# Kernel optimization log

Measured on AMD Instinct MI355X. Metric: run time of the kernel, lower is better.

## Reference

```python
import jax, jax.numpy as jnp
import numpy as np
import math

DIM, DEPTH, HEADS, VOCAB, DMODEL = 200, 6, 10, 7, 512
DH = DIM // HEADS                      # 20
NBF = int(DH * math.log(DH))           # 59 FAVOR+ random features
FF = 4 * DIM                           # 800


def setup_inputs() -> dict:
    key = jax.random.key(0)
    ks = iter(jax.random.split(key, 32))
    s = 0.02
    inp = {
        'x': jax.random.normal(next(ks), (4, 16, 2048), jnp.float32),
        'token_emb': jax.random.normal(next(ks), (VOCAB, DIM)) * s,
        'ln1_g': jnp.ones((DEPTH, DIM)), 'ln1_b': jnp.zeros((DEPTH, DIM)),
        'wq': jax.random.normal(next(ks), (DEPTH, DIM, DIM)) * s, 'bq': jnp.zeros((DEPTH, DIM)),
        'wk': jax.random.normal(next(ks), (DEPTH, DIM, DIM)) * s, 'bk': jnp.zeros((DEPTH, DIM)),
        'wv': jax.random.normal(next(ks), (DEPTH, DIM, DIM)) * s, 'bv': jnp.zeros((DEPTH, DIM)),
        'proj': jax.random.normal(next(ks), (DEPTH, NBF, DH)),  # FAVOR+ projection (buffer)
        'wo': jax.random.normal(next(ks), (DEPTH, DIM, DIM)) * s, 'bo': jnp.zeros((DEPTH, DIM)),
        'ln2_g': jnp.ones((DEPTH, DIM)), 'ln2_b': jnp.zeros((DEPTH, DIM)),
        'ffw1': jax.random.normal(next(ks), (DEPTH, DIM, FF)) * s, 'ffb1': jnp.zeros((DEPTH, FF)),
        'ffw2': jax.random.normal(next(ks), (DEPTH, FF, DIM)) * s, 'ffb2': jnp.zeros((DEPTH, DIM)),
        'lnf_g': jnp.ones((DIM,)), 'lnf_b': jnp.zeros((DIM,)),
        'proj_w': jax.random.normal(next(ks), (DIM, DMODEL)) * s, 'proj_b': jnp.zeros((DMODEL,)),
    }
    return inp


def layer_norm(x, g, b, eps=1e-5):
    mu = x.mean(-1, keepdims=True)
    var = ((x - mu) ** 2).mean(-1, keepdims=True)
    return (x - mu) / jnp.sqrt(var + eps) * g + b


def softmax_kernel(data, proj, is_query, eps=1e-4):
    # data: (N,H,S,dh); proj: (m,dh)
    dn = data * (data.shape[-1] ** -0.25)
    dash = jnp.einsum('nhsd,md->nhsm', dn, proj)
    diag = 0.5 * jnp.sum(dn * dn, axis=-1, keepdims=True)
    mx = jnp.max(dash, axis=-1, keepdims=True) if is_query else jnp.max(dash)
    return (proj.shape[0] ** -0.5) * (jnp.exp(dash - diag - mx) + eps)


def attention(x, wq, bq, wk, bk, wv, bv, proj, wo, bo):
    N, S, D = x.shape
    split = lambda t: t.reshape(N, S, HEADS, DH).transpose(0, 2, 1, 3)
    q, k, v = split(x @ wq + bq), split(x @ wk + bk), split(x @ wv + bv)
    qp = softmax_kernel(q, proj, True)
    kp = softmax_kernel(k, proj, False)
    d_inv = 1.0 / jnp.einsum('nhsm,nhm->nhs', qp, kp.sum(axis=2))
    ctx = jnp.einsum('nhsm,nhsd->nhmd', kp, v)          # linear attention context
    out = jnp.einsum('nhsm,nhmd->nhsd', qp, ctx) * d_inv[..., None]
    return out.transpose(0, 2, 1, 3).reshape(N, S, D) @ wo + bo


def feedforward(x, w1, b1, w2, b2):
    return jax.nn.gelu(x @ w1 + b1, approximate=False) @ w2 + b2


def performer_forward(tokens, p):
    h = p['token_emb'][tokens]            # pos_emb is zeros (g2v_position_emb=False)
    x1, x2 = h, h                         # reversible net: x duplicated along channels
    for l in range(DEPTH):
        x1 = x1 + attention(layer_norm(x2, p['ln1_g'][l], p['ln1_b'][l]),
                            p['wq'][l], p['bq'][l], p['wk'][l], p['bk'][l],
                            p['wv'][l], p['bv'][l], p['proj'][l], p['wo'][l], p['bo'][l])
        x2 = x2 + feedforward(layer_norm(x1, p['ln2_g'][l], p['ln2_b'][l]),
                              p['ffw1'][l], p['ffb1'][l], p['ffw2'][l], p['ffb2'][l])
    h = 0.5 * (x1 + x2)                   # mean over the two reversible halves
    return layer_norm(h, p['lnf_g'], p['lnf_b'])


def reference(x, token_emb, ln1_g, ln1_b, wq, bq, wk, bk, wv, bv, proj, wo, bo,
              ln2_g, ln2_b, ffw1, ffb1, ffw2, ffb2, lnf_g, lnf_b, proj_w, proj_b):
    p = dict(token_emb=token_emb, ln1_g=ln1_g, ln1_b=ln1_b, wq=wq, bq=bq, wk=wk, bk=bk,
             wv=wv, bv=bv, proj=proj, wo=wo, bo=bo, ln2_g=ln2_g, ln2_b=ln2_b,
             ffw1=ffw1, ffb1=ffb1, ffw2=ffw2, ffb2=ffb2, lnf_g=lnf_g, lnf_b=lnf_b)
    B, Nt, T = x.shape
    xf = x.reshape(B * Nt, T)
    # torch.quantile on 1D positives -> bin_edges shape (1,4) != (T,4), so the
    # original falls back to zero bin edges; edges_plus = [0,0,0,0,inf], hence
    # token = 4 if value > 0 else 0, then + cls_token_id (1).
    tokens = jnp.where(xf > 0, 4, 0).astype(jnp.int32) + 1
    # chunk loop (chunk_size=512 samples) is identity math: run all at once
    enc = performer_forward(tokens, p)    # (B*Nt, T, DIM)
    pooled = enc.mean(axis=1)             # mean-pool over sequence
    out = pooled @ proj_w + proj_b
    return out.reshape(B, Nt, DMODEL)
```

## Files before the change

kernel.cpp:

```cpp
#include <hip/hip_runtime.h>
#include <hip/hip_bf16.h>
#include <math.h>

#define DEPTH   6
#define DIM     200
#define HEADS   10
#define DH      20
#define NBF     59
#define FFD     800
#define DMODEL  512
#define NSEQ    64
#define SEQ     2048
#define NTOK    (NSEQ*SEQ)
#define KPAD    224
#define BUFPAD  64
#define KNROW   40
#define VROW    136
#define KPROW   136
#define QPROW   72
#define CTXR    21
#define HSROW   132
#define PKV_E   (512*KPAD)
#define PQ_E    (256*KPAD)
#define PWO_E   (256*KPAD)
#define PF1_E   (896*KPAD)
#define PF2_E   (256*800)

typedef __hip_bfloat16 bf16;
typedef unsigned short u16;
typedef short s8v __attribute__((ext_vector_type(8)));
typedef short s4v __attribute__((ext_vector_type(4)));
typedef float f4v __attribute__((ext_vector_type(4)));

constexpr float SCALE = 0.4728708045015879f;
constexpr float RATIO = 0.1301889109808239f;
constexpr float KEPS  = 1e-4f;

__device__ __forceinline__ float b2f(bf16 v) { return __bfloat162float(v); }
__device__ __forceinline__ bf16 f2b(float v) { return __float2bfloat16(v); }
__device__ __forceinline__ float bfu(u16 u) {
    return __uint_as_float(((unsigned)u) << 16);
}
__device__ __forceinline__ u16 f2u(float v) {
    bf16 hb = __float2bfloat16(v);
    return *(u16*)&hb;
}
__device__ __forceinline__ float gelu_f(float x) {
    float inner = 0.7978845608028654f * (x + 0.044715f * x * x * x);
    float e = __expf(2.f * inner);
    return x * (1.f - 1.f / (e + 1.f));
}
__device__ __forceinline__ void gld_lds16(const short* g, short* l) {
    __builtin_amdgcn_global_load_lds(
        (const __attribute__((address_space(1))) void*)g,
        (__attribute__((address_space(3))) void*)l, 16, 0, 0);
}
#define MFMA16(a, b, c) __builtin_amdgcn_mfma_f32_16x16x32_bf16(a, b, c, 0, 0, 0)

__global__ void sentinel_kernel(float* out, float wsmb) {
    if (threadIdx.x == 0) out[0] = wsmb;
}

__global__ void zeropad_kernel(bf16* p1, bf16* p2, bf16* p3, bf16* p4) {
    int i = threadIdx.x;
    if (i < BUFPAD) {
        bf16 z = f2b(0.f);
        p1[i] = z; p2[i] = z; p3[i] = z; p4[i] = z;
    }
}

__global__ __launch_bounds__(256) void prep_layer(
        const float* __restrict__ wq, const float* __restrict__ wk,
        const float* __restrict__ wv, const float* __restrict__ wo,
        const float* __restrict__ f1, const float* __restrict__ f2,
        const float* __restrict__ g1, const float* __restrict__ b1,
        const float* __restrict__ g2, const float* __restrict__ b2,
        const float* __restrict__ bq, const float* __restrict__ bk,
        const float* __restrict__ bv, const float* __restrict__ f1b,
        bf16* __restrict__ pKV, bf16* __restrict__ pQ, bf16* __restrict__ pWO,
        bf16* __restrict__ pF1, bf16* __restrict__ pF2,
        float* __restrict__ uw) {
    int b = blockIdx.x, t = threadIdx.x;
    if (b < 448) {
        int idx = b * 256 + t;
        int row = idx / KPAD, k = idx % KPAD;
        float v = 0.f;
        if (k < DIM) {
            if (row < DIM) v = wk[(size_t)k * DIM + row] * g1[k];
            else if (row >= 256 && row < 256 + DIM)
                v = wv[(size_t)k * DIM + (row - 256)] * g1[k];
        }
        pKV[idx] = f2b(v);
    } else if (b < 672) {
        int idx = (b - 448) * 256 + t;
        int row = idx / KPAD, k = idx % KPAD;
        float v = (row < DIM && k < DIM) ? wq[(size_t)k * DIM + row] * g1[k] : 0.f;
        pQ[idx] = f2b(v);
    } else if (b < 896) {
        int idx = (b - 672) * 256 + t;
        int row = idx / KPAD, k = idx % KPAD;
        float v = (row < DIM && k < DIM) ? wo[(size_t)k * DIM + row] : 0.f;
        pWO[idx] = f2b(v);
    } else if (b < 1680) {
        int idx = (b - 896) * 256 + t;
        int row = idx / KPAD, k = idx % KPAD;
        float v = (row < FFD && k < DIM) ? f1[(size_t)k * FFD + row] * g2[k] : 0.f;
        pF1[idx] = f2b(v);
    } else if (b < 2480) {
        int idx = (b - 1680) * 256 + t;
        int row = idx / 800, k = idx % 800;
        float v = (row < DIM) ? f2[(size_t)k * DIM + row] : 0.f;
        pF2[idx] = f2b(v);
    } else if (b < 2482) {
        int j = b - 2480;
        const float* W    = j ? wv : wk;
        const float* bias = j ? bv : bk;
        int n = t;
        float su = 0.f, sw = 0.f;
        if (n < DIM) {
            for (int k = 0; k < DIM; ++k) {
                float wvv = W[(size_t)k * DIM + n];
                su += g1[k] * wvv;
                sw += b1[k] * wvv;
            }
            sw += bias[n];
        }
        uw[j * 256 + n] = su;
        uw[512 + j * 256 + n] = sw;
    } else if (b == 2482) {
        int n = t;
        float su = 0.f, sw = 0.f;
        if (n < DIM) {
            for (int k = 0; k < DIM; ++k) {
                float wvv = wq[(size_t)k * DIM + n];
                su += g1[k] * wvv;
                sw += b1[k] * wvv;
            }
            sw += bq[n];
        }
        uw[1024 + n] = su;
        uw[1280 + n] = sw;
    } else {
        int n = (b - 2483) * 256 + t;
        if (n < 896) {
            float su = 0.f, sw = 0.f;
            if (n < FFD) {
                for (int k = 0; k < DIM; ++k) {
                    float wvv = f1[(size_t)k * FFD + n];
                    su += g2[k] * wvv;
                    sw += b2[k] * wvv;
                }
                sw += f1b[n];
            }
            uw[1536 + n] = su;
            uw[2432 + n] = sw;
        }
    }
}

__global__ __launch_bounds__(256) void embed_kernel(const float* __restrict__ x,
        const float* __restrict__ emb, bf16* __restrict__ x1, bf16* __restrict__ x2) {
    int idx = blockIdx.x * 256 + threadIdx.x;
    if (idx >= NTOK * 25) return;
    int t = idx / 25, c = idx % 25;
    int row = (x[t] > 0.f) ? 5 : 1;
    const float4* e4 = (const float4*)(emb + row * DIM + c * 8);
    float4 e0 = e4[0], e1 = e4[1];
    s8v o;
    o[0] = (short)f2u(e0.x); o[1] = (short)f2u(e0.y);
    o[2] = (short)f2u(e0.z); o[3] = (short)f2u(e0.w);
    o[4] = (short)f2u(e1.x); o[5] = (short)f2u(e1.y);
    o[6] = (short)f2u(e1.z); o[7] = (short)f2u(e1.w);
    size_t off = (size_t)t * DIM + c * 8;
    *(s8v*)((short*)x1 + off) = o;
    *(s8v*)((short*)x2 + off) = o;
}

__global__ __launch_bounds__(256) void lnstats_kernel(const bf16* __restrict__ in,
        float* __restrict__ mu_o, float* __restrict__ rstd_o) {
    int lane = threadIdx.x & 63;
    size_t t = (size_t)blockIdx.x * 4 + (threadIdx.x >> 6);
    const u16* row = (const u16*)in + t * DIM;
    float v0 = 0.f, v1 = 0.f, v2 = 0.f, v3 = 0.f;
    if (lane < 50) {
        ushort4 u4 = ((const ushort4*)row)[lane];
        v0 = bfu(u4.x); v1 = bfu(u4.y); v2 = bfu(u4.z); v3 = bfu(u4.w);
    }
    float s = v0 + v1 + v2 + v3, qq = v0*v0 + v1*v1 + v2*v2 + v3*v3;
    #pragma unroll
    for (int o = 32; o > 0; o >>= 1) { s += __shfl_xor(s, o); qq += __shfl_xor(qq, o); }
    if (lane == 0) {
        float mu = s * (1.f / DIM);
        mu_o[t] = mu;
        rstd_o[t] = rsqrtf(qq * (1.f / DIM) - mu * mu + 1e-5f);
    }
}

__global__ __launch_bounds__(256) void finalln_kernel(const bf16* __restrict__ in1,
        const bf16* __restrict__ in2, const float* __restrict__ g,
        const float* __restrict__ b, bf16* __restrict__ out) {
    int lane = threadIdx.x & 63;
    size_t t = (size_t)blockIdx.x * 4 + (threadIdx.x >> 6);
    const u16* r1 = (const u16*)in1 + t * DIM;
    const u16* r2 = (const u16*)in2 + t * DIM;
    float v0 = 0.f, v1 = 0.f, v2 = 0.f, v3 = 0.f;
    if (lane < 50) {
        ushort4 a4 = ((const ushort4*)r1)[lane];
        ushort4 b4 = ((const ushort4*)r2)[lane];
        v0 = 0.5f * (bfu(a4.x) + bfu(b4.x));
        v1 = 0.5f * (bfu(a4.y) + bfu(b4.y));
        v2 = 0.5f * (bfu(a4.z) + bfu(b4.z));
        v3 = 0.5f * (bfu(a4.w) + bfu(b4.w));
    }
    float s = v0 + v1 + v2 + v3, qq = v0*v0 + v1*v1 + v2*v2 + v3*v3;
    #pragma unroll
    for (int o = 32; o > 0; o >>= 1) { s += __shfl_xor(s, o); qq += __shfl_xor(qq, o); }
    float mu = s * (1.f / DIM);
    float rstd = rsqrtf(qq * (1.f / DIM) - mu * mu + 1e-5f);
    if (lane < 50) {
        float4 g4 = ((const float4*)g)[lane];
        float4 b4f = ((const float4*)b)[lane];
        ushort4 o4;
        o4.x = f2u((v0 - mu) * rstd * g4.x + b4f.x);
        o4.y = f2u((v1 - mu) * rstd * g4.y + b4f.y);
        o4.z = f2u((v2 - mu) * rstd * g4.z + b4f.z);
        o4.w = f2u((v3 - mu) * rstd * g4.w + b4f.w);
        ((ushort4*)((u16*)out + t * DIM))[lane] = o4;
    }
}

template<int EPI, int LNE, int KV>
__global__ __launch_bounds__(256) void gemm_m(
        const bf16* __restrict__ A, const bf16* __restrict__ Bt,
        const float* __restrict__ wv_, const float* __restrict__ uv_,
        const float* __restrict__ mu, const float* __restrict__ rstd,
        bf16* __restrict__ C, bf16* __restrict__ C2,
        int M, int N, int K, int Kpad) {
    __shared__ __align__(16) short As[128 * 32];
    __shared__ __align__(16) short Bs[128 * 32];
    int bm = blockIdx.x * 128, bn = blockIdx.y * 128;
    int t = threadIdx.x, l = t & 63, w = t >> 6;
    int wr = (w >> 1) * 64, wc = (w & 1) * 64;
    int lr = l & 15, lk16 = l >> 4;
    f4v acc[4][4];
    #pragma unroll
    for (int i = 0; i < 4; ++i)
        #pragma unroll
        for (int j = 0; j < 4; ++j) acc[i][j] = (f4v){0.f, 0.f, 0.f, 0.f};

    const short* Ash = (const short*)A;
    const short* Bsh = (const short*)Bt;
    int srow0 = 32 * w + (l >> 2);
    int c16 = l & 3;
    for (int k0 = 0; k0 < Kpad; k0 += 32) {
        __syncthreads();
        #pragma unroll
        for (int j = 0; j < 2; ++j) {
            int row = srow0 + 16 * j;
            int xc = (c16 ^ ((row >> 1) & 3)) * 8;
            gld_lds16(Ash + (size_t)(bm + row) * K + k0 + xc,
                      &As[(32 * w + 16 * j) * 32]);
            gld_lds16(Bsh + (size_t)(bn + row) * Kpad + k0 + xc,
                      &Bs[(32 * w + 16 * j) * 32]);
        }
        __syncthreads();
        s8v a[4], b[4];
        #pragma unroll
        for (int fi = 0; fi < 4; ++fi) {
            int R = wr + fi * 16 + lr;
            a[fi] = *(const s8v*)&As[R * 32 + ((lk16 ^ ((R >> 1) & 3)) * 8)];
        }
        #pragma unroll
        for (int fj = 0; fj < 4; ++fj) {
            int R = wc + fj * 16 + lr;
            b[fj] = *(const s8v*)&Bs[R * 32 + ((lk16 ^ ((R >> 1) & 3)) * 8)];
        }
        #pragma unroll
        for (int fi = 0; fi < 4; ++fi)
            #pragma unroll
            for (int fj = 0; fj < 4; ++fj)
                acc[fi][fj] = MFMA16(a[fi], b[fj], acc[fi][fj]);
    }
    int r0 = (l >> 4) * 4;
    #pragma unroll
    for (int fi = 0; fi < 4; ++fi) {
        int rowb = bm + wr + fi * 16 + r0;
        float sr[4] = {1.f, 1.f, 1.f, 1.f}, tr[4] = {0.f, 0.f, 0.f, 0.f};
        if (LNE) {
            #pragma unroll
            for (int r = 0; r < 4; ++r) {
                sr[r] = rstd[rowb + r];
                tr[r] = mu[rowb + r] * sr[r];
            }
        }
        #pragma unroll
        for (int fj = 0; fj < 4; ++fj) {
            int col = bn + wc + fj * 16 + lr;
            if (KV) {
                int cc = col & 255;
                if (cc < DIM) {
                    bf16* dst = (col < 256) ? C : C2;
                    float ww = wv_[col], uu = uv_[col];
                    #pragma unroll
                    for (int r = 0; r < 4; ++r) {
                        size_t idx = (size_t)(rowb + r) * DIM + cc;
                        float v = sr[r] * acc[fi][fj][r] - tr[r] * uu + ww;
                        dst[idx] = f2b(v);
                    }
                }
            } else if (col < N) {
                float ww = wv_[col];
                float uu = LNE ? uv_[col] : 0.f;
                #pragma unroll
                for (int r = 0; r < 4; ++r) {
                    size_t idx = (size_t)(rowb + r) * N + col;
                    float v = LNE ? (sr[r] * acc[fi][fj][r] - tr[r] * uu + ww)
                                  : (acc[fi][fj][r] + ww);
                    if (EPI == 1) v += b2f(C[idx]);
                    if (EPI == 2) v = gelu_f(v);
                    C[idx] = f2b(v);
                }
            }
        }
    }
}

__global__ __launch_bounds__(256, 2) void ff_fused(
        const bf16* __restrict__ x1, const bf16* __restrict__ pF1,
        const bf16* __restrict__ pF2, const float* __restrict__ u1,
        const float* __restrict__ w1f, const float* __restrict__ fb2,
        const float* __restrict__ mu_in, const float* __restrict__ rstd_in,
        float* __restrict__ mu_out, float* __restrict__ rstd_out,
        bf16* __restrict__ x2) {
    __shared__ __align__(16) short Ax[64 * 256];
    __shared__ __align__(16) short Bs[2 * 128 * 32];
    __shared__ __align__(16) short hS[64 * HSROW];
    int bm = blockIdx.x * 64;
    int t = threadIdx.x, l = t & 63, w = t >> 6;
    int wrA = (w >> 1) * 32;
    int wcA = (w & 1) * 64;
    int wcB = (w & 1) * 128;
    int lr = l & 15, lk16 = l >> 4;
    int r0 = (l >> 4) * 4;
    const short* X1 = (const short*)x1;
    const short* F1 = (const short*)pF1;
    const short* F2 = (const short*)pF2;

    {
        int c = l & 31, rsub = l >> 5;
        #pragma unroll
        for (int j = 0; j < 8; ++j) {
            int row0 = w * 16 + j * 2;
            int row = row0 + rsub;
            gld_lds16(X1 + (size_t)(bm + row) * DIM + ((c ^ (row & 7)) * 8),
                      &Ax[row0 * 256]);
        }
    }

    f4v acc2[2][8];
    #pragma unroll
    for (int i = 0; i < 2; ++i)
        #pragma unroll
        for (int j = 0; j < 8; ++j) acc2[i][j] = (f4v){0.f, 0.f, 0.f, 0.f};

    int srow0 = 32 * w + (l >> 2);
    int c16 = l & 3;
    #pragma unroll 1
    for (int hc = 0; hc < 7; ++hc) {
        __syncthreads();
        #pragma unroll
        for (int j = 0; j < 2; ++j) {
            int row = srow0 + 16 * j;
            int xc = (c16 ^ ((row >> 1) & 3)) * 8;
            gld_lds16(F1 + (size_t)(hc * 128 + row) * KPAD + 0 + xc,
                      &Bs[(32 * w + 16 * j) * 32]);
        }
        __syncthreads();
        f4v acc1[2][4];
        #pragma unroll
        for (int i = 0; i < 2; ++i)
            #pragma unroll
            for (int j = 0; j < 4; ++j) acc1[i][j] = (f4v){0.f, 0.f, 0.f, 0.f};
        #pragma unroll 1
        for (int kt = 0; kt < 7; ++kt) {
            if (kt < 6) {
                int k0n = (kt + 1) * 32;
                int hb = ((kt + 1) & 1) * 4096;
                #pragma unroll
                for (int j = 0; j < 2; ++j) {
                    int row = srow0 + 16 * j;
                    int xc = (c16 ^ ((row >> 1) & 3)) * 8;
                    gld_lds16(F1 + (size_t)(hc * 128 + row) * KPAD + k0n + xc,
                              &Bs[hb + (32 * w + 16 * j) * 32]);
                }
            }
            int hb = (kt & 1) * 4096;
            s8v a[2], b[4];
            int cg = kt * 4 + lk16;
            #pragma unroll
            for (int fi = 0; fi < 2; ++fi) {
                int R = wrA + fi * 16 + lr;
                a[fi] = *(const s8v*)&Ax[R * 256 + ((cg ^ (R & 7)) * 8)];
            }
            #pragma unroll
            for (int fj = 0; fj < 4; ++fj) {
                int R = wcA + fj * 16 + lr;
                b[fj] = *(const s8v*)&Bs[hb + R * 32 + ((lk16 ^ ((R >> 1) & 3)) * 8)];
            }
            #pragma unroll
            for (int fi = 0; fi < 2; ++fi)
                #pragma unroll
                for (int fj = 0; fj < 4; ++fj)
                    acc1[fi][fj] = MFMA16(a[fi], b[fj], acc1[fi][fj]);
            __syncthreads();
        }
        #pragma unroll
        for (int fi = 0; fi < 2; ++fi) {
            int rowL = wrA + fi * 16 + r0;
            f4v rs = *(const f4v*)&rstd_in[bm + rowL];
            f4v mm = *(const f4v*)&mu_in[bm + rowL];
            #pragma unroll
            for (int fj = 0; fj < 4; ++fj) {
                int col = wcA + fj * 16 + lr;
                int gcol = hc * 128 + col;
                float uu = u1[gcol], ww = w1f[gcol];
                #pragma unroll
                for (int r = 0; r < 4; ++r) {
                    float v = rs[r] * acc1[fi][fj][r] - mm[r] * rs[r] * uu + ww;
                    v = gelu_f(v);
                    int rr = rowL + r;
                    hS[rr * HSROW + (((col >> 3) ^ (rr & 7)) * 8) + (col & 7)]
                        = (short)f2u(v);
                }
            }
        }
        #pragma unroll 1
        for (int ks = 0; ks < 4; ++ks) {
            __syncthreads();
            #pragma unroll
            for (int j = 0; j < 4; ++j) {
                int row = (w * 4 + j) * 16 + (l >> 2);
                int xc = (c16 ^ ((row >> 1) & 3)) * 8;
                gld_lds16(F2 + (size_t)row * 800 + hc * 128 + ks * 32 + xc,
                          &Bs[(w * 4 + j) * 16 * 32]);
            }
            __syncthreads();
            s8v a[2];
            int cg = ks * 4 + lk16;
            #pragma unroll
            for (int fi = 0; fi < 2; ++fi) {
                int R = wrA + fi * 16 + lr;
                a[fi] = *(const s8v*)&hS[R * HSROW + ((cg ^ (R & 7)) * 8)];
            }
            #pragma unroll
            for (int fj = 0; fj < 8; ++fj) {
                int Br = wcB + fj * 16 + lr;
                s8v bfr = *(const s8v*)&Bs[Br * 32 + ((lk16 ^ ((Br >> 1) & 3)) * 8)];
                #pragma unroll
                for (int fi = 0; fi < 2; ++fi)
                    acc2[fi][fj] = MFMA16(a[fi], bfr, acc2[fi][fj]);
            }
        }
    }
    __syncthreads();
    float* sp = (float*)hS;
    float rsum[2][4], rsq[2][4];
    #pragma unroll
    for (int fi = 0; fi < 2; ++fi)
        #pragma unroll
        for (int r = 0; r < 4; ++r) { rsum[fi][r] = 0.f; rsq[fi][r] = 0.f; }
    #pragma unroll
    for (int fi = 0; fi < 2; ++fi) {
        int rowb = bm + wrA + fi * 16 + r0;
        #pragma unroll
        for (int fj = 0; fj < 8; ++fj) {
            int col = wcB + fj * 16 + lr;
            if (col < DIM) {
                float bb = fb2[col];
                #pragma unroll
                for (int r = 0; r < 4; ++r) {
                    size_t idx = (size_t)(rowb + r) * DIM + col;
                    float v = acc2[fi][fj][r] + bb + b2f(x2[idx]);
                    x2[idx] = f2b(v);
                    rsum[fi][r] += v;
                    rsq[fi][r] += v * v;
                }
            }
        }
    }
    #pragma unroll
    for (int fi = 0; fi < 2; ++fi)
        #pragma unroll
        for (int r = 0; r < 4; ++r) {
            float s = rsum[fi][r], q = rsq[fi][r];
            #pragma unroll
            for (int o = 8; o > 0; o >>= 1) {
                s += __shfl_xor(s, o);
                q += __shfl_xor(q, o);
            }
            rsum[fi][r] = s; rsq[fi][r] = q;
        }
    if (lr == 0) {
        #pragma unroll
        for (int fi = 0; fi < 2; ++fi)
            #pragma unroll
            for (int r = 0; r < 4; ++r) {
                int rowL = wrA + fi * 16 + r0 + r;
                sp[rowL * 4 + (w & 1) * 2 + 0] = rsum[fi][r];
                sp[rowL * 4 + (w & 1) * 2 + 1] = rsq[fi][r];
            }
    }
    __syncthreads();
    if (t < 64) {
        float s = sp[t * 4 + 0] + sp[t * 4 + 2];
        float q = sp[t * 4 + 1] + sp[t * 4 + 3];
        float mu = s * (1.f / DIM);
        mu_out[bm + t] = mu;
        rstd_out[bm + t] = rsqrtf(q * (1.f / DIM) - mu * mu + 1e-5f);
    }
}

__global__ __launch_bounds__(256) void kvctx_mfma(const bf16* __restrict__ k,
        const bf16* __restrict__ v, const float* __restrict__ proj,
        float* __restrict__ ctxg) {
    __shared__ __align__(16) short ph[64 * KNROW];
    __shared__ __align__(16) short pl[64 * KNROW];
    __shared__ __align__(16) short knh[128 * KNROW];
    __shared__ __align__(16) short knl[128 * KNROW];
    __shared__ __align__(16) short vT[32 * VROW];
    __shared__ __align__(16) short kp[64 * KPROW];
    __shared__ __align__(16) float diag[128];
    __shared__ float wmax[4];
    int nh = blockIdx.x, n = nh / HEADS, h = nh % HEADS;
    int t = threadIdx.x, l = t & 63, w = t >> 6;
    int lr = l & 15, lk = (l >> 4) * 8, l4 = (l >> 4) * 4;
    for (int i = t; i < 64 * 32; i += 256) {
        int m = i >> 5, d = i & 31;
        float val = (m < NBF && d < DH) ? proj[m * DH + d] : 0.f;
        u16 hi = f2u(val);
        ph[m * KNROW + d] = (short)hi;
        pl[m * KNROW + d] = (short)f2u(val - bfu(hi));
    }
    for (int i = t; i < 128 * 12; i += 256) {
        int s = i / 12, d = 20 + i % 12;
        knh[s * KNROW + d] = 0; knl[s * KNROW + d] = 0;
    }
    for (int i = t; i < 12 * 128; i += 256) {
        int d = 20 + (i >> 7), s = i & 127;
        vT[d * VROW + s] = (short)((d == 20) ? f2u(1.0f) : 0);
    }
    s8v ones;
    #pragma unroll
    for (int i = 0; i < 8; ++i) ones[i] = (short)f2u(1.0f);
    float Mrun = -3.0e38f;
    f4v cd0 = {0.f,0.f,0.f,0.f}, cd1 = {0.f,0.f,0.f,0.f};
    f4v vs0 = {0.f,0.f,0.f,0.f}, vs1 = {0.f,0.f,0.f,0.f};
    for (int c = 0; c < 16; ++c) {
        int s0 = c * 128;
        __syncthreads();
        if (t < 128) {
            int s = t;
            const u16* kr = (const u16*)k + ((size_t)(n * SEQ + s0 + s)) * DIM + h * DH;
            float dg = 0.f;
            #pragma unroll
            for (int q5 = 0; q5 < 5; ++q5) {
                ushort4 u4 = ((const ushort4*)kr)[q5];
                float f0 = bfu(u4.x) * SCALE, f1 = bfu(u4.y) * SCALE;
                float f2_ = bfu(u4.z) * SCALE, f3 = bfu(u4.w) * SCALE;
                dg += f0*f0 + f1*f1 + f2_*f2_ + f3*f3;
                u16 h0 = f2u(f0), h1 = f2u(f1), h2 = f2u(f2_), h3 = f2u(f3);
                s4v hv = {(short)h0, (short)h1, (short)h2, (short)h3};
                *(s4v*)&knh[s * KNROW + q5 * 4] = hv;
                s4v lv = {(short)f2u(f0 - bfu(h0)), (short)f2u(f1 - bfu(h1)),
                          (short)f2u(f2_ - bfu(h2)), (short)f2u(f3 - bfu(h3))};
                *(s4v*)&knl[s * KNROW + q5 * 4] = lv;
            }
            diag[s] = 0.5f * dg;
        } else {
            int s = t - 128;
            const u16* vr = (const u16*)v + ((size_t)(n * SEQ + s0 + s)) * DIM + h * DH;
            #pragma unroll
            for (int q5 = 0; q5 < 5; ++q5) {
                ushort4 u4 = ((const ushort4*)vr)[q5];
                vT[(q5 * 4 + 0) * VROW + s] = (short)u4.x;
                vT[(q5 * 4 + 1) * VROW + s] = (short)u4.y;
                vT[(q5 * 4 + 2) * VROW + s] = (short)u4.z;
                vT[(q5 * 4 + 3) * VROW + s] = (short)u4.w;
            }
        }
        __syncthreads();
        s8v ah0 = *(const s8v*)&knh[(32 * w + lr) * KNROW + lk];
        s8v al0 = *(const s8v*)&knl[(32 * w + lr) * KNROW + lk];
        s8v ah1 = *(const s8v*)&knh[(32 * w + 16 + lr) * KNROW + lk];
        s8v al1 = *(const s8v*)&knl[(32 * w + 16 + lr) * KNROW + lk];
        f4v dg0 = *(const f4v*)&diag[32 * w + l4];
        f4v dg1 = *(const f4v*)&diag[32 * w + 16 + l4];
        f4v D0[4], D1[4];
        #pragma unroll
        for (int mt = 0; mt < 4; ++mt) {
            s8v bh = *(const s8v*)&ph[(mt * 16 + lr) * KNROW + lk];
            s8v bl = *(const s8v*)&pl[(mt * 16 + lr) * KNROW + lk];
            f4v d0 = {0.f, 0.f, 0.f, 0.f}, d1 = {0.f, 0.f, 0.f, 0.f};
            d0 = MFMA16(ah0, bh, d0); d0 = MFMA16(ah0, bl, d0); d0 = MFMA16(al0, bh, d0);
            d1 = MFMA16(ah1, bh, d1); d1 = MFMA16(ah1, bl, d1); d1 = MFMA16(al1, bh, d1);
            D0[mt] = d0; D1[mt] = d1;
        }
        float mm = -3.0e38f;
        #pragma unroll
        for (int mt = 0; mt < 4; ++mt) {
            int lim = (mt < 3) ? 16 : (NBF - 48);
            if (lr < lim) {
                #pragma unroll
                for (int r = 0; r < 4; ++r)
                    mm = fmaxf(mm, fmaxf(D0[mt][r], D1[mt][r]));
            }
        }
        #pragma unroll
        for (int o = 32; o > 0; o >>= 1) mm = fmaxf(mm, __shfl_xor(mm, o));
        if (l == 0) wmax[w] = mm;
        __syncthreads();
        float Mnew = fmaxf(fmaxf(wmax[0], wmax[1]), fmaxf(wmax[2], wmax[3]));
        Mnew = fmaxf(Mrun, Mnew);
        float scl = __expf(Mrun - Mnew);
        #pragma unroll
        for (int r = 0; r < 4; ++r) { cd0[r] *= scl; cd1[r] *= scl; }
        Mrun = Mnew;
        #pragma unroll
        for (int mt = 0; mt < 4; ++mt) {
            int m = mt * 16 + lr;
            bool valid = m < NBF;
            s4v o0, o1;
            #pragma unroll
            for (int r = 0; r < 4; ++r) {
                float kp0 = valid ? __expf(D0[mt][r] - dg0[r] - Mnew) : 0.f;
                float kp1 = valid ? __expf(D1[mt][r] - dg1[r] - Mnew) : 0.f;
                o0[r] = (short)f2u(kp0);
                o1[r] = (short)f2u(kp1);
            }
            *(s4v*)&kp[m * KPROW + 32 * w + l4] = o0;
            *(s4v*)&kp[m * KPROW + 32 * w + 16 + l4] = o1;
        }
        __syncthreads();
        #pragma unroll
        for (int ks = 0; ks < 4; ++ks) {
            s8v a  = *(const s8v*)&kp[(16 * w + lr) * KPROW + ks * 32 + lk];
            s8v b0 = *(const s8v*)&vT[lr * VROW + ks * 32 + lk];
            s8v b1 = *(const s8v*)&vT[(16 + lr) * VROW + ks * 32 + lk];
            cd0 = MFMA16(a, b0, cd0);
            cd1 = MFMA16(a, b1, cd1);
            vs0 = MFMA16(ones, b0, vs0);
            vs1 = MFMA16(ones, b1, vs1);
        }
    }
    float* cg = ctxg + (size_t)nh * CTXR * 64;
    int m0 = 16 * w + l4;
    f4v r0v, r1v;
    #pragma unroll
    for (int r = 0; r < 4; ++r) {
        r0v[r] = RATIO * (cd0[r] + KEPS * vs0[r]);
        r1v[r] = RATIO * (cd1[r] + KEPS * vs1[r]);
    }
    *(f4v*)&cg[lr * 64 + m0] = r0v;
    if (lr < 5) *(f4v*)&cg[(16 + lr) * 64 + m0] = r1v;
}

__global__ __launch_bounds__(256) void qattn_mfma(const bf16* __restrict__ q,
        const float* __restrict__ proj, const float* __restrict__ ctxg,
        bf16* __restrict__ ao) {
    __shared__ __align__(16) short ph[64 * KNROW];
    __shared__ __align__(16) short pl[64 * KNROW];
    __shared__ __align__(16) short qnh[128 * KNROW];
    __shared__ __align__(16) short qnl[128 * KNROW];
    __shared__ __align__(16) short qp[128 * QPROW];
    __shared__ __align__(16) short cT[32 * QPROW];
    __shared__ __align__(16) float dgs[128];
    __shared__ __align__(16) float osf[128][22];
    int b = blockIdx.x;
    int nh = b >> 2, sc = b & 3;
    int n = nh / HEADS, h = nh % HEADS;
    int t = threadIdx.x, l = t & 63, w = t >> 6;
    int lr = l & 15, lk = (l >> 4) * 8, l4 = (l >> 4) * 4;
    for (int i = t; i < 64 * 32; i += 256) {
        int m = i >> 5, d = i & 31;
        float val = (m < NBF && d < DH) ? proj[m * DH + d] : 0.f;
        u16 hi = f2u(val);
        ph[m * KNROW + d] = (short)hi;
        pl[m * KNROW + d] = (short)f2u(val - bfu(hi));
    }
    for (int i = t; i < 128 * 12; i += 256) {
        int s = i / 12, d = 20 + i % 12;
        qnh[s * KNROW + d] = 0; qnl[s * KNROW + d] = 0;
    }
    for (int i = t; i < 32 * 64; i += 256) {
        int d = i >> 6, m = i & 63;
        float val = (d < CTXR) ? ctxg[(size_t)nh * CTXR * 64 + d * 64 + m] : 0.f;
        cT[d * QPROW + m] = (short)f2u(val);
    }
    for (int c = 0; c < 4; ++c) {
        int s0 = (sc * 4 + c) * 128;
        __syncthreads();
        if (t < 128) {
            int s = t;
            const u16* qr = (const u16*)q + ((size_t)(n * SEQ + s0 + s)) * DIM + h * DH;
            float dg = 0.f;
            #pragma unroll
            for (int q5 = 0; q5 < 5; ++q5) {
                ushort4 u4 = ((const ushort4*)qr)[q5];
                float f0 = bfu(u4.x) * SCALE, f1 = bfu(u4.y) * SCALE;
                float f2_ = bfu(u4.z) * SCALE, f3 = bfu(u4.w) * SCALE;
                dg += f0*f0 + f1*f1 + f2_*f2_ + f3*f3;
                u16 h0 = f2u(f0), h1 = f2u(f1), h2 = f2u(f2_), h3 = f2u(f3);
                s4v hv = {(short)h0, (short)h1, (short)h2, (short)h3};
                *(s4v*)&qnh[s * KNROW + q5 * 4] = hv;
                s4v lv = {(short)f2u(f0 - bfu(h0)), (short)f2u(f1 - bfu(h1)),
                          (short)f2u(f2_ - bfu(h2)), (short)f2u(f3 - bfu(h3))};
                *(s4v*)&qnl[s * KNROW + q5 * 4] = lv;
            }
            dgs[s] = 0.5f * dg;
        }
        __syncthreads();
        s8v ah0 = *(const s8v*)&qnh[(32 * w + lr) * KNROW + lk];
        s8v al0 = *(const s8v*)&qnl[(32 * w + lr) * KNROW + lk];
        s8v ah1 = *(const s8v*)&qnh[(32 * w + 16 + lr) * KNROW + lk];
        s8v al1 = *(const s8v*)&qnl[(32 * w + 16 + lr) * KNROW + lk];
        f4v D0[4], D1[4];
        #pragma unroll
        for (int mt = 0; mt < 4; ++mt) {
            s8v bh = *(const s8v*)&ph[(mt * 16 + lr) * KNROW + lk];
            s8v bl = *(const s8v*)&pl[(mt * 16 + lr) * KNROW + lk];
            f4v d0 = {0.f, 0.f, 0.f, 0.f}, d1 = {0.f, 0.f, 0.f, 0.f};
            d0 = MFMA16(ah0, bh, d0); d0 = MFMA16(ah0, bl, d0); d0 = MFMA16(al0, bh, d0);
            d1 = MFMA16(ah1, bh, d1); d1 = MFMA16(ah1, bl, d1); d1 = MFMA16(al1, bh, d1);
            D0[mt] = d0; D1[mt] = d1;
        }
        f4v dg0 = *(const f4v*)&dgs[32 * w + l4];
        f4v dg1 = *(const f4v*)&dgs[32 * w + 16 + l4];
        float mx0[4], mx1[4];
        #pragma unroll
        for (int r = 0; r < 4; ++r) {
            float v3 = (lr < NBF - 48) ? D0[3][r] : -3.4e38f;
            float mm = fmaxf(fmaxf(D0[0][r], D0[1][r]), fmaxf(D0[2][r], v3));
            mm = fmaxf(mm, __shfl_xor(mm, 1));
            mm = fmaxf(mm, __shfl_xor(mm, 2));
            mm = fmaxf(mm, __shfl_xor(mm, 4));
            mm = fmaxf(mm, __shfl_xor(mm, 8));
            mx0[r] = mm;
            float u3 = (lr < NBF - 48) ? D1[3][r] : -3.4e38f;
            float nn = fmaxf(fmaxf(D1[0][r], D1[1][r]), fmaxf(D1[2][r], u3));
            nn = fmaxf(nn, __shfl_xor(nn, 1));
            nn = fmaxf(nn, __shfl_xor(nn, 2));
            nn = fmaxf(nn, __shfl_xor(nn, 4));
            nn = fmaxf(nn, __shfl_xor(nn, 8));
            mx1[r] = nn;
        }
        #pragma unroll
        for (int mt = 0; mt < 4; ++mt) {
            int m = mt * 16 + lr;
            bool valid = m < NBF;
            #pragma unroll
            for (int r = 0; r < 4; ++r) {
                float p0 = valid ? RATIO * (__expf(D0[mt][r] - dg0[r] - mx0[r]) + KEPS) : 0.f;
                float p1 = valid ? RATIO * (__expf(D1[mt][r] - dg1[r] - mx1[r]) + KEPS) : 0.f;
                qp[(32 * w + l4 + r) * QPROW + m] = (short)f2u(p0);
                qp[(32 * w + 16 + l4 + r) * QPROW + m] = (short)f2u(p1);
            }
        }
        __syncthreads();
        f4v o00 = {0.f,0.f,0.f,0.f}, o01 = {0.f,0.f,0.f,0.f};
        f4v o10 = {0.f,0.f,0.f,0.f}, o11 = {0.f,0.f,0.f,0.f};
        #pragma unroll
        for (int ks = 0; ks < 2; ++ks) {
            s8v a0 = *(const s8v*)&qp[(32 * w + lr) * QPROW + ks * 32 + lk];
            s8v a1 = *(const s8v*)&qp[(32 * w + 16 + lr) * QPROW + ks * 32 + lk];
            s8v b0 = *(const s8v*)&cT[lr * QPROW + ks * 32 + lk];
            s8v b1 = *(const s8v*)&cT[(16 + lr) * QPROW + ks * 32 + lk];
            o00 = MFMA16(a0, b0, o00); o01 = MFMA16(a0, b1, o01);
            o10 = MFMA16(a1, b0, o10); o11 = MFMA16(a1, b1, o11);
        }
        #pragma unroll
        for (int r = 0; r < 4; ++r) {
            osf[32 * w + l4 + r][lr] = o00[r];
            osf[32 * w + 16 + l4 + r][lr] = o10[r];
            if (lr < 5) {
                osf[32 * w + l4 + r][16 + lr] = o01[r];
                osf[32 * w + 16 + l4 + r][16 + lr] = o11[r];
            }
        }
        __syncthreads();
        if (t < 128) osf[t][21] = 1.f / osf[t][20];
        __syncthreads();
        int tokb = n * SEQ + s0;
        for (int idx = t; idx < 128 * 10; idx += 256) {
            int row = idx / 10, seg = idx % 10;
            float di = osf[row][21];
            ushort2 o2;
            o2.x = f2u(osf[row][seg * 2] * di);
            o2.y = f2u(osf[row][seg * 2 + 1] * di);
            *(ushort2*)((u16*)ao + (size_t)(tokb + row) * DIM + h * DH + seg * 2) = o2;
        }
    }
}

__global__ __launch_bounds__(256) void pool1_kernel(const bf16* __restrict__ hn,
        float* __restrict__ partial) {
    int n = blockIdx.x / 16, c = blockIdx.x % 16;
    int d = threadIdx.x;
    if (d >= DIM) return;
    float acc = 0.f;
    const bf16* base = hn + ((size_t)n * SEQ + c * 128) * DIM + d;
    for (int s = 0; s < 128; ++s) acc += b2f(base[(size_t)s * DIM]);
    partial[(size_t)blockIdx.x * DIM + d] = acc;
}

__global__ __launch_bounds__(256) void pool2_kernel(const float* __restrict__ partial,
        float* __restrict__ pooled) {
    int n = blockIdx.x, d = threadIdx.x;
    if (d >= DIM) return;
    float acc = 0.f;
    for (int c = 0; c < 16; ++c) acc += partial[(size_t)(n * 16 + c) * DIM + d];
    pooled[n * DIM + d] = acc * (1.f / SEQ);
}

__global__ __launch_bounds__(512) void finalproj_kernel(const float* __restrict__ pooled,
        const float* __restrict__ pw, const float* __restrict__ pb,
        float* __restrict__ out) {
    __shared__ float ps[DIM];
    int n = blockIdx.x;
    for (int i = threadIdx.x; i < DIM; i += 512) ps[i] = pooled[n * DIM + i];
    __syncthreads();
    int j = threadIdx.x;
    float acc = pb[j];
    for (int d = 0; d < DIM; ++d) acc += ps[d] * pw[d * DMODEL + j];
    out[n * DMODEL + j] = acc;
}

extern "C" void kernel_launch(void* const* d_in, const int* in_sizes, int n_in,
                              void* d_out, int out_size, void* d_ws, size_t ws_size,
                              hipStream_t stream) {
    (void)in_sizes; (void)n_in; (void)out_size;
    const float* x    = (const float*)d_in[0];
    const float* emb  = (const float*)d_in[1];
    const float* ln1g = (const float*)d_in[2];
    const float* ln1b = (const float*)d_in[3];
    const float* wq   = (const float*)d_in[4];
    const float* bq   = (const float*)d_in[5];
    const float* wk   = (const float*)d_in[6];
    const float* bk   = (const float*)d_in[7];
    const float* wv   = (const float*)d_in[8];
    const float* bv   = (const float*)d_in[9];
    const float* proj = (const float*)d_in[10];
    const float* wo   = (const float*)d_in[11];
    const float* bo   = (const float*)d_in[12];
    const float* ln2g = (const float*)d_in[13];
    const float* ln2b = (const float*)d_in[14];
    const float* ffw1 = (const float*)d_in[15];
    const float* ffb1 = (const float*)d_in[16];
    const float* ffw2 = (const float*)d_in[17];
    const float* ffb2 = (const float*)d_in[18];
    const float* lnfg = (const float*)d_in[19];
    const float* lnfb = (const float*)d_in[20];
    const float* pw   = (const float*)d_in[21];
    const float* pb   = (const float*)d_in[22];
    float* out = (float*)d_out;

    const size_t A_ = (size_t)NTOK * DIM;
    bf16* x1 = (bf16*)d_ws;
    bf16* x2 = x1 + A_ + BUFPAD;
    bf16* b3 = x2 + A_ + BUFPAD;
    bf16* b4 = b3 + A_ + BUFPAD;
    bf16* pKV = b4 + A_ + BUFPAD;
    bf16* pQ  = pKV + PKV_E;
    bf16* pWO = pQ + PQ_E;
    bf16* pF1 = pWO + PWO_E;
    bf16* pF2 = pF1 + PF1_E;
    float* muB   = (float*)(pF2 + PF2_E);
    float* rstdB = muB + NTOK;
    float* muC   = rstdB + NTOK;
    float* rstdC = muC + NTOK;
    float* uw    = rstdC + NTOK;
    float* ctxg  = uw + 3328;
    float* wsend = ctxg + (size_t)NSEQ * HEADS * CTXR * 64;

    float* ukv = uw,        *wkv = uw + 512;
    float* uq  = uw + 1024, *wqf = uw + 1280;
    float* u1  = uw + 1536, *w1f = uw + 2432;

    size_t need = (char*)wsend - (char*)d_ws;
    if (ws_size < need) {
        sentinel_kernel<<<1, 64, 0, stream>>>(out, (float)(ws_size >> 20));
        return;
    }

    zeropad_kernel<<<1, 64, 0, stream>>>(x1 + A_, x2 + A_, b3 + A_, b4 + A_);
    embed_kernel<<<(NTOK * 25 + 255) / 256, 256, 0, stream>>>(x, emb, x1, x2);
    lnstats_kernel<<<NTOK / 4, 256, 0, stream>>>(x2, muB, rstdB);

    dim3 gkv(NTOK / 128, 4);
    dim3 gd(NTOK / 128, 2);
    for (int l = 0; l < DEPTH; ++l) {
        const float* wq_l = wq + (size_t)l * DIM * DIM;
        const float* wk_l = wk + (size_t)l * DIM * DIM;
        const float* wv_l = wv + (size_t)l * DIM * DIM;
        const float* wo_l = wo + (size_t)l * DIM * DIM;
        const float* f1_l = ffw1 + (size_t)l * DIM * FFD;
        const float* f2_l = ffw2 + (size_t)l * FFD * DIM;
        const float* pj_l = proj + (size_t)l * NBF * DH;
        const float* g1 = ln1g + l * DIM, *b1 = ln1b + l * DIM;
        const float* g2 = ln2g + l * DIM, *b2 = ln2b + l * DIM;

        prep_layer<<<2487, 256, 0, stream>>>(wq_l, wk_l, wv_l, wo_l, f1_l, f2_l,
                g1, b1, g2, b2, bq + l * DIM, bk + l * DIM, bv + l * DIM,
                ffb1 + l * FFD, pKV, pQ, pWO, pF1, pF2, uw);

        gemm_m<0, 1, 1><<<gkv, 256, 0, stream>>>(x2, pKV, wkv, ukv, muB, rstdB,
                b3, b4, NTOK, 512, DIM, KPAD);
        kvctx_mfma<<<NSEQ * HEADS, 256, 0, stream>>>(b3, b4, pj_l, ctxg);
        gemm_m<0, 1, 0><<<gd, 256, 0, stream>>>(x2, pQ, wqf, uq, muB, rstdB,
                b3, nullptr, NTOK, DIM, DIM, KPAD);
        qattn_mfma<<<NSEQ * HEADS * 4, 256, 0, stream>>>(b3, pj_l, ctxg, b4);
        gemm_m<1, 0, 0><<<gd, 256, 0, stream>>>(b4, pWO, bo + l * DIM, nullptr,
                nullptr, nullptr, x1, nullptr, NTOK, DIM, DIM, KPAD);

        lnstats_kernel<<<NTOK / 4, 256, 0, stream>>>(x1, muC, rstdC);
        ff_fused<<<NTOK / 64, 256, 0, stream>>>(x1, pF1, pF2, u1, w1f,
                ffb2 + l * DIM, muC, rstdC, muB, rstdB, x2);
    }

    finalln_kernel<<<NTOK / 4, 256, 0, stream>>>(x1, x2, lnfg, lnfb, b3);
    float* partial = muB;
    float* pooled  = muB + (size_t)NSEQ * 16 * DIM;
    pool1_kernel<<<NSEQ * 16, 256, 0, stream>>>(b3, partial);
    pool2_kernel<<<NSEQ, 256, 0, stream>>>(partial, pooled);
    finalproj_kernel<<<NSEQ, 512, 0, stream>>>(pooled, pw, pb, out);
}
```

Before: 4.327 ms.

## Store Q/K/V head-major and prefetch first FF2 weight tile before GELU epilogue

The Q and K/V projection GEMM epilogues now write their outputs in a head-major layout [head][token][DH] instead of token-major [token][DIM]. The attention kernels (kvctx and qattn) read each head's rows contiguously, which replaces 40-byte strided reads per token with dense reads. Separately, ff_fused issues the first FF2 weight tile load before the GELU epilogue writes to shared memory, so that load overlaps with the epilogue and one barrier is removed. The cost is more scattered, narrower stores in the GEMM epilogues plus integer divide/mod work for the head index.

```diff
diff --git a/kernel.cpp b/kernel.cpp
--- a/kernel.cpp
+++ b/kernel.cpp
@@ -20,6 +20,7 @@
 #define QPROW   72
 #define CTXR    21
 #define HSROW   132
+#define HSTRIDE ((size_t)NTOK * DH)
 #define PKV_E   (512*KPAD)
 #define PQ_E    (256*KPAD)
 #define PWO_E   (256*KPAD)
@@ -229,7 +230,7 @@
     }
 }
 
-template<int EPI, int LNE, int KV>
+template<int EPI, int LNE, int KV, int HB>
 __global__ __launch_bounds__(256) void gemm_m(
         const bf16* __restrict__ A, const bf16* __restrict__ Bt,
         const float* __restrict__ wv_, const float* __restrict__ uv_,
@@ -300,10 +301,12 @@
                 int cc = col & 255;
                 if (cc < DIM) {
                     bf16* dst = (col < 256) ? C : C2;
+                    int hh = cc / DH, dd = cc % DH;
+                    size_t base = (size_t)hh * HSTRIDE + dd;
                     float ww = wv_[col], uu = uv_[col];
                     #pragma unroll
                     for (int r = 0; r < 4; ++r) {
-                        size_t idx = (size_t)(rowb + r) * DIM + cc;
+                        size_t idx = base + (size_t)(rowb + r) * DH;
                         float v = sr[r] * acc[fi][fj][r] - tr[r] * uu + ww;
                         dst[idx] = f2b(v);
                     }
@@ -313,7 +316,13 @@
                 float uu = LNE ? uv_[col] : 0.f;
                 #pragma unroll
                 for (int r = 0; r < 4; ++r) {
-                    size_t idx = (size_t)(rowb + r) * N + col;
+                    size_t idx;
+                    if (HB) {
+                        int hh = col / DH, dd = col % DH;
+                        idx = (size_t)hh * HSTRIDE + (size_t)(rowb + r) * DH + dd;
+                    } else {
+                        idx = (size_t)(rowb + r) * N + col;
+                    }
                     float v = LNE ? (sr[r] * acc[fi][fj][r] - tr[r] * uu + ww)
                                   : (acc[fi][fj][r] + ww);
                     if (EPI == 1) v += b2f(C[idx]);
@@ -415,6 +424,13 @@
             __syncthreads();
         }
         #pragma unroll
+        for (int j = 0; j < 4; ++j) {
+            int row = (w * 4 + j) * 16 + (l >> 2);
+            int xc = (c16 ^ ((row >> 1) & 3)) * 8;
+            gld_lds16(F2 + (size_t)row * 800 + hc * 128 + 0 + xc,
+                      &Bs[(w * 4 + j) * 16 * 32]);
+        }
+        #pragma unroll
         for (int fi = 0; fi < 2; ++fi) {
             int rowL = wrA + fi * 16 + r0;
             f4v rs = *(const f4v*)&rstd_in[bm + rowL];
@@ -436,13 +452,15 @@
         }
         #pragma unroll 1
         for (int ks = 0; ks < 4; ++ks) {
-            __syncthreads();
-            #pragma unroll
-            for (int j = 0; j < 4; ++j) {
-                int row = (w * 4 + j) * 16 + (l >> 2);
-                int xc = (c16 ^ ((row >> 1) & 3)) * 8;
-                gld_lds16(F2 + (size_t)row * 800 + hc * 128 + ks * 32 + xc,
-                          &Bs[(w * 4 + j) * 16 * 32]);
+            if (ks) {
+                __syncthreads();
+                #pragma unroll
+                for (int j = 0; j < 4; ++j) {
+                    int row = (w * 4 + j) * 16 + (l >> 2);
+                    int xc = (c16 ^ ((row >> 1) & 3)) * 8;
+                    gld_lds16(F2 + (size_t)row * 800 + hc * 128 + ks * 32 + xc,
+                              &Bs[(w * 4 + j) * 16 * 32]);
+                }
             }
             __syncthreads();
             s8v a[2];
@@ -534,6 +552,8 @@
     int nh = blockIdx.x, n = nh / HEADS, h = nh % HEADS;
     int t = threadIdx.x, l = t & 63, w = t >> 6;
     int lr = l & 15, lk = (l >> 4) * 8, l4 = (l >> 4) * 4;
+    const u16* kbase = (const u16*)k + (size_t)h * HSTRIDE;
+    const u16* vbase = (const u16*)v + (size_t)h * HSTRIDE;
     for (int i = t; i < 64 * 32; i += 256) {
         int m = i >> 5, d = i & 31;
         float val = (m < NBF && d < DH) ? proj[m * DH + d] : 0.f;
@@ -560,7 +580,7 @@
         __syncthreads();
         if (t < 128) {
             int s = t;
-            const u16* kr = (const u16*)k + ((size_t)(n * SEQ + s0 + s)) * DIM + h * DH;
+            const u16* kr = kbase + (size_t)(n * SEQ + s0 + s) * DH;
             float dg = 0.f;
             #pragma unroll
             for (int q5 = 0; q5 < 5; ++q5) {
@@ -578,7 +598,7 @@
             diag[s] = 0.5f * dg;
         } else {
             int s = t - 128;
-            const u16* vr = (const u16*)v + ((size_t)(n * SEQ + s0 + s)) * DIM + h * DH;
+            const u16* vr = vbase + (size_t)(n * SEQ + s0 + s) * DH;
             #pragma unroll
             for (int q5 = 0; q5 < 5; ++q5) {
                 ushort4 u4 = ((const ushort4*)vr)[q5];
@@ -680,6 +700,7 @@
     int n = nh / HEADS, h = nh % HEADS;
     int t = threadIdx.x, l = t & 63, w = t >> 6;
     int lr = l & 15, lk = (l >> 4) * 8, l4 = (l >> 4) * 4;
+    const u16* qbase = (const u16*)q + (size_t)h * HSTRIDE;
     for (int i = t; i < 64 * 32; i += 256) {
         int m = i >> 5, d = i & 31;
         float val = (m < NBF && d < DH) ? proj[m * DH + d] : 0.f;
@@ -701,7 +722,7 @@
         __syncthreads();
         if (t < 128) {
             int s = t;
-            const u16* qr = (const u16*)q + ((size_t)(n * SEQ + s0 + s)) * DIM + h * DH;
+            const u16* qr = qbase + (size_t)(n * SEQ + s0 + s) * DH;
             float dg = 0.f;
             #pragma unroll
             for (int q5 = 0; q5 < 5; ++q5) {
@@ -912,13 +933,13 @@
                 g1, b1, g2, b2, bq + l * DIM, bk + l * DIM, bv + l * DIM,
                 ffb1 + l * FFD, pKV, pQ, pWO, pF1, pF2, uw);
 
-        gemm_m<0, 1, 1><<<gkv, 256, 0, stream>>>(x2, pKV, wkv, ukv, muB, rstdB,
+        gemm_m<0, 1, 1, 0><<<gkv, 256, 0, stream>>>(x2, pKV, wkv, ukv, muB, rstdB,
                 b3, b4, NTOK, 512, DIM, KPAD);
         kvctx_mfma<<<NSEQ * HEADS, 256, 0, stream>>>(b3, b4, pj_l, ctxg);
-        gemm_m<0, 1, 0><<<gd, 256, 0, stream>>>(x2, pQ, wqf, uq, muB, rstdB,
+        gemm_m<0, 1, 0, 1><<<gd, 256, 0, stream>>>(x2, pQ, wqf, uq, muB, rstdB,
                 b3, nullptr, NTOK, DIM, DIM, KPAD);
         qattn_mfma<<<NSEQ * HEADS * 4, 256, 0, stream>>>(b3, pj_l, ctxg, b4);
-        gemm_m<1, 0, 0><<<gd, 256, 0, stream>>>(b4, pWO, bo + l * DIM, nullptr,
+        gemm_m<1, 0, 0, 0><<<gd, 256, 0, stream>>>(b4, pWO, bo + l * DIM, nullptr,
                 nullptr, nullptr, x1, nullptr, NTOK, DIM, DIM, KPAD);
 
         lnstats_kernel<<<NTOK / 4, 256, 0, stream>>>(x1, muC, rstdC);
```

Measured after the change: 4.198 ms. 1.03x faster.
